# Performance work log

Measured on AMD Instinct MI355X. Metric: run time of the kernel, lower is better.

Reference implementation:

```python
import jax, jax.numpy as jnp
import numpy as np

EMBED_DIM = 1024
NUM_HEADS = 16
N_POS = 2048
BATCH = 4


def setup_inputs() -> dict:
    key = jax.random.key(0)
    k_x, k_w1, k_b1, k_wo, k_bo = jax.random.split(key, 5)
    s1 = 1.0 / np.sqrt(EMBED_DIM)
    x = jax.random.normal(k_x, (BATCH, N_POS, EMBED_DIM), dtype=jnp.float32)
    # torch Linear weights stored as [in, out] for x @ W + b
    W_qkv = jax.random.uniform(k_w1, (EMBED_DIM, 3 * EMBED_DIM), dtype=jnp.float32, minval=-s1, maxval=s1)
    b_qkv = jax.random.uniform(k_b1, (3 * EMBED_DIM,), dtype=jnp.float32, minval=-s1, maxval=s1)
    W_o = jax.random.uniform(k_wo, (EMBED_DIM, EMBED_DIM), dtype=jnp.float32, minval=-s1, maxval=s1)
    b_o = jax.random.uniform(k_bo, (EMBED_DIM,), dtype=jnp.float32, minval=-s1, maxval=s1)
    return {"x": x, "W_qkv": W_qkv, "b_qkv": b_qkv, "W_o": W_o, "b_o": b_o}


def reference(x, W_qkv, b_qkv, W_o, b_o):
    B, N, C = x.shape
    H = NUM_HEADS
    d_k = C // H
    qkv = x @ W_qkv + b_qkv                       # [B, N, 3C]
    q, k, v = jnp.split(qkv, 3, axis=-1)
    q = q.reshape(B, N, H, d_k).transpose(0, 2, 1, 3)  # [B, H, N, d_k]
    k = k.reshape(B, N, H, d_k).transpose(0, 2, 1, 3)
    v = v.reshape(B, N, H, d_k).transpose(0, 2, 1, 3)
    scores = jnp.einsum('bhqd,bhkd->bhqk', q, k) * (1.0 / np.sqrt(d_k))
    causal = jnp.tril(jnp.ones((N, N), dtype=bool))
    scores = jnp.where(causal, scores, -jnp.inf)
    attn = jax.nn.softmax(scores, axis=-1)
    out = jnp.einsum('bhqk,bhkd->bhqd', attn, v)  # [B, H, N, d_k]
    out = out.transpose(0, 2, 1, 3).reshape(B, N, C)
    return out @ W_o + b_o
```

## Files before the change

kernel.cpp:

```cpp
#include <hip/hip_runtime.h>
#include <hip/hip_bf16.h>

typedef __attribute__((ext_vector_type(8))) __bf16 bf16x8;
typedef __attribute__((ext_vector_type(4))) float f32x4;
typedef __attribute__((ext_vector_type(16))) float f32x16;
typedef __attribute__((ext_vector_type(4))) unsigned short u16x4;
typedef __attribute__((ext_vector_type(8))) unsigned short u16x8;
typedef unsigned short u16;

#define MFMA16 __builtin_amdgcn_mfma_f32_16x16x32_bf16
#define MFMA32 __builtin_amdgcn_mfma_f32_32x32x16_bf16

#if __has_builtin(__builtin_amdgcn_exp2f)
#define EXP2F __builtin_amdgcn_exp2f
#else
#define EXP2F(x) __expf((x) * 0.69314718056f)
#endif

__device__ inline u16 f32_to_bf16_bits(float f) {
    unsigned u = __builtin_bit_cast(unsigned, f);
    unsigned r = u + 0x7FFFu + ((u >> 16) & 1u);
    return (u16)(r >> 16);
}
__device__ inline u16 f32_to_bf16_fast(float f) {
    unsigned u = __builtin_bit_cast(unsigned, f);
    return (u16)((u + 0x8000u) >> 16);
}

__device__ inline void g2l16(const void* g, void* l) {
    __builtin_amdgcn_global_load_lds(
        (const __attribute__((address_space(1))) unsigned int*)g,
        (__attribute__((address_space(3))) unsigned int*)l,
        16, 0, 0);
}

__global__ void cvt_bf16_kernel(const float* __restrict__ in, u16* __restrict__ out, int n) {
    int i = (blockIdx.x * 256 + threadIdx.x) * 4;
    if (i >= n) return;
    f32x4 v = *(const f32x4*)&in[i];
    u16x4 r;
#pragma unroll
    for (int j = 0; j < 4; ++j) r[j] = f32_to_bf16_bits(v[j]);
    *(u16x4*)&out[i] = r;
}

__global__ __launch_bounds__(256) void cvt_t_kernel(const float* __restrict__ W,
                                                    u16* __restrict__ WT, int K, int N) {
    const int w = threadIdx.x >> 6, l = threadIdx.x & 63;
    const int n = blockIdx.x * 64 + l;
    const int k0 = blockIdx.y * 32 + w * 8;
    u16x8 r;
#pragma unroll
    for (int i = 0; i < 8; ++i)
        r[i] = f32_to_bf16_bits(W[(size_t)(k0 + i) * N + n]);
    *(u16x8*)&WT[(size_t)n * K + k0] = r;
}

template <int STORE_BF16>
__global__ __launch_bounds__(256) void gemm_nt(
    const u16* __restrict__ A, const u16* __restrict__ BT,
    const float* __restrict__ bias, void* __restrict__ Cv,
    int M, int N, int K, int qcols, float qscale)
{
    __shared__ __align__(16) u16 As[128 * 64];
    __shared__ __align__(16) u16 Bs[128 * 64];
    const int tid = threadIdx.x;
    const int w = tid >> 6, l = tid & 63;
    const int lr = l & 15, lh = l >> 4;
    const int wr = (w >> 1) * 64, wc = (w & 1) * 64;
    const int m0 = blockIdx.y * 128, n0 = blockIdx.x * 128;

    f32x4 acc[4][4];
#pragma unroll
    for (int m = 0; m < 4; ++m)
#pragma unroll
        for (int n = 0; n < 4; ++n) acc[m][n] = (f32x4)(0.0f);

    for (int k0 = 0; k0 < K; k0 += 64) {
        __syncthreads();
#pragma unroll
        for (int p = 0; p < 4; ++p) {
            int f = p * 256 + tid;
            int r = f >> 3, kk = (f & 7) << 3;
            g2l16(A + (size_t)(m0 + r) * K + (k0 + kk), &As[(p * 4 + w) * 512]);
            g2l16(BT + (size_t)(n0 + r) * K + (k0 + kk), &Bs[(p * 4 + w) * 512]);
        }
        __syncthreads();
#pragma unroll
        for (int ks = 0; ks < 2; ++ks) {
            bf16x8 af[4], bfr[4];
#pragma unroll
            for (int m = 0; m < 4; ++m)
                af[m] = *(const bf16x8*)&As[(wr + m * 16 + lr) * 64 + ks * 32 + lh * 8];
#pragma unroll
            for (int n = 0; n < 4; ++n)
                bfr[n] = *(const bf16x8*)&Bs[(wc + n * 16 + lr) * 64 + ks * 32 + lh * 8];
#pragma unroll
            for (int m = 0; m < 4; ++m)
#pragma unroll
                for (int n = 0; n < 4; ++n)
                    acc[m][n] = MFMA16(af[m], bfr[n], acc[m][n], 0, 0, 0);
        }
    }

#pragma unroll
    for (int m = 0; m < 4; ++m) {
        int row = m0 + wr + m * 16 + lh * 4;
#pragma unroll
        for (int n = 0; n < 4; ++n) {
            int col = n0 + wc + n * 16 + lr;
            float bs = bias[col];
            float sc = (col < qcols) ? qscale : 1.0f;
#pragma unroll
            for (int j = 0; j < 4; ++j) {
                float v = (acc[m][n][j] + bs) * sc;
                if (STORE_BF16)
                    ((u16*)Cv)[(size_t)(row + j) * N + col] = f32_to_bf16_bits(v);
                else
                    ((float*)Cv)[(size_t)(row + j) * N + col] = v;
            }
        }
    }
}

__global__ __launch_bounds__(512, 2) void attn_kernel(
    const u16* __restrict__ qkv, u16* __restrict__ ctx)
{
    __shared__ __align__(16) u16 SM[32768];

    const int bid = blockIdx.x;
    const int xcd = bid & 7, jj = bid >> 3;
    const int bh = xcd * 8 + (jj >> 2);
    const int pr = jj & 3;
    const int b = bh >> 4, h = bh & 15;
    const size_t rowbase = (size_t)b * 2048;
    const int tid = threadIdx.x, w = tid >> 6, l = tid & 63;
    const int lq = l & 31, lk = l >> 5;
    u16* const PL = SM + 16384 + w * 2048;

    const int rstage = w * 8 + (l >> 3);
    const int cstage = l & 7;
    const int kchunk = cstage ^ (l >> 3);

    bf16x8 vreg;

#pragma unroll
    for (int pass = 0; pass < 2; ++pass) {
        const int qt = pass ? (7 - pr) : pr;
        const int q0 = qt * 256;
        const int nt = 4 * qt + 4;
        const int qbase = q0 + w * 32;

        const u16* qp = qkv + (rowbase + qbase + lq) * 3072 + h * 64 + lk * 8;
        bf16x8 qf[4];
#pragma unroll
        for (int j = 0; j < 4; ++j) qf[j] = *(const bf16x8*)(qp + j * 16);

        f32x16 ot[2];
#pragma unroll
        for (int dt = 0; dt < 2; ++dt) ot[dt] = (f32x16)(0.0f);
        float m_run = -3e38f, l_run = 0.0f;

        __syncthreads();
        g2l16(qkv + (rowbase + rstage) * 3072 + 1024 + h * 64 + kchunk * 8, SM + w * 512);
        vreg = *(const bf16x8*)(qkv + (rowbase + rstage) * 3072 + 2048 + h * 64 + cstage * 8);
        asm volatile("s_waitcnt vmcnt(0)" ::: "memory");
#pragma unroll
        for (int i = 0; i < 8; ++i) {
            const int d = cstage * 8 + i;
            SM[8192 + (((d * 64 + rstage) ^ (((i ^ cstage) & 7) << 3)))] = ((const u16*)&vreg)[i];
        }
        __syncthreads();

        for (int t = 0; t < nt; ++t) {
            const int c = t & 1;
            const int kb = t * 64;
            u16* const Kb = SM + (c ? 4096 : 0);
            u16* const Vb = SM + 8192 + (c ? 4096 : 0);

            if (t + 1 < nt) {
                const int kb2 = kb + 64;
                g2l16(qkv + (rowbase + kb2 + rstage) * 3072 + 1024 + h * 64 + kchunk * 8,
                      SM + (c ? 0 : 4096) + w * 512);
                vreg = *(const bf16x8*)(qkv + (rowbase + kb2 + rstage) * 3072 + 2048 + h * 64 + cstage * 8);
            }

            if (kb <= qbase + 31) {
                bf16x8 kf[2][4];
#pragma unroll
                for (int kt = 0; kt < 2; ++kt)
#pragma unroll
                    for (int j = 0; j < 4; ++j)
                        kf[kt][j] = *(const bf16x8*)&Kb[((kt * 32 + lq) * 64 + j * 16 + lk * 8) ^ ((lq & 7) << 3)];

                f32x16 sf[2];
                __builtin_amdgcn_s_setprio(1);
#pragma unroll
                for (int kt = 0; kt < 2; ++kt) {
                    f32x16 z = (f32x16)(0.0f);
#pragma unroll
                    for (int j = 0; j < 4; ++j) z = MFMA32(kf[kt][j], qf[j], z, 0, 0, 0);
                    sf[kt] = z;
                }
                __builtin_amdgcn_s_setprio(0);

                float mt = -3e38f;
                if (kb + 63 > qbase) {
                    const int qrow = qbase + lq;
#pragma unroll
                    for (int kt = 0; kt < 2; ++kt)
#pragma unroll
                        for (int r = 0; r < 16; ++r) {
                            const int key = kb + kt * 32 + (r & 3) + 8 * (r >> 2) + 4 * lk;
                            float v = sf[kt][r];
                            if (key > qrow) v = -3e38f;
                            sf[kt][r] = v;
                            mt = fmaxf(mt, v);
                        }
                } else {
#pragma unroll
                    for (int kt = 0; kt < 2; ++kt)
#pragma unroll
                        for (int r = 0; r < 16; ++r) mt = fmaxf(mt, sf[kt][r]);
                }
                mt = fmaxf(mt, __shfl_xor(mt, 32));

                const bool defer = __all(mt <= m_run + 16.0f);
                float mn = m_run;
                if (!defer) {
                    mn = fmaxf(m_run, mt);
                    const float alpha = EXP2F(m_run - mn);
                    m_run = mn;
                    l_run *= alpha;
#pragma unroll
                    for (int dt = 0; dt < 2; ++dt)
#pragma unroll
                        for (int r = 0; r < 16; ++r) ot[dt][r] *= alpha;
                }
                float rs = 0.0f;
#pragma unroll
                for (int kt = 0; kt < 2; ++kt)
#pragma unroll
                    for (int r = 0; r < 16; ++r) {
                        const float pp = EXP2F(sf[kt][r] - mn);
                        sf[kt][r] = pp;
                        rs += pp;
                    }
                rs += __shfl_xor(rs, 32);
                l_run += rs;

#pragma unroll
                for (int kt = 0; kt < 2; ++kt)
#pragma unroll
                    for (int rg = 0; rg < 4; ++rg) {
                        u16x4 pk;
#pragma unroll
                        for (int j2 = 0; j2 < 4; ++j2) pk[j2] = f32_to_bf16_fast(sf[kt][rg * 4 + j2]);
                        *(u16x4*)&PL[((lq * 64) + (kt * 32 + rg * 8 + lk * 4)) ^ ((lq & 7) << 3)] = pk;
                    }

                __builtin_amdgcn_s_setprio(1);
#pragma unroll
                for (int k0 = 0; k0 < 4; ++k0) {
                    const bf16x8 pb = *(const bf16x8*)&PL[((lq * 64) + (k0 * 16 + lk * 8)) ^ ((lq & 7) << 3)];
#pragma unroll
                    for (int dt = 0; dt < 2; ++dt) {
                        const int d = dt * 32 + lq;
                        const int vswz = ((d & 7) ^ (d >> 3)) & 7;
                        const bf16x8 vf = *(const bf16x8*)&Vb[((d * 64) + (k0 * 16 + lk * 8)) ^ (vswz << 3)];
                        ot[dt] = MFMA32(vf, pb, ot[dt], 0, 0, 0);
                    }
                }
                __builtin_amdgcn_s_setprio(0);
            }

            asm volatile("s_waitcnt vmcnt(0)" ::: "memory");
            if (t + 1 < nt) {
                u16* const Vn = SM + 8192 + (c ? 0 : 4096);
#pragma unroll
                for (int i = 0; i < 8; ++i) {
                    const int d = cstage * 8 + i;
                    Vn[((d * 64 + rstage) ^ (((i ^ cstage) & 7) << 3))] = ((const u16*)&vreg)[i];
                }
            }
            __syncthreads();
        }

        u16* const out_l = SM + w * 2176;
        const float inv = 1.0f / l_run;
#pragma unroll
        for (int dt = 0; dt < 2; ++dt)
#pragma unroll
            for (int r = 0; r < 16; ++r) {
                const int d = dt * 32 + (r & 3) + 8 * (r >> 2) + 4 * lk;
                out_l[lq * 68 + d] = f32_to_bf16_bits(ot[dt][r] * inv);
            }
#pragma unroll
        for (int rr = 0; rr < 4; ++rr) {
            const int row = rr * 8 + (l >> 3);
            const bf16x8 v = *(const bf16x8*)&out_l[row * 68 + (l & 7) * 8];
            *(bf16x8*)(ctx + (rowbase + qbase + row) * 1024 + h * 64 + (l & 7) * 8) = v;
        }
    }
}

extern "C" void kernel_launch(void* const* d_in, const int* in_sizes, int n_in,
                              void* d_out, int out_size, void* d_ws, size_t ws_size,
                              hipStream_t stream) {
    const float* x      = (const float*)d_in[0];
    const float* W_qkv  = (const float*)d_in[1];
    const float* b_qkv  = (const float*)d_in[2];
    const float* W_o    = (const float*)d_in[3];
    const float* b_o    = (const float*)d_in[4];
    float* out = (float*)d_out;

    const int M = 4 * 2048;
    const int C = 1024;
    u16* qkv   = (u16*)d_ws;
    u16* xb    = qkv   + (size_t)M * 3 * C;
    u16* wqkvt = xb    + (size_t)M * C;
    u16* ctx   = wqkvt + (size_t)3 * C * C;
    u16* wot   = ctx   + (size_t)M * C;

    const float SCQ = 0.125f * 1.44269504089f;

    cvt_bf16_kernel<<<(M * C) / (256 * 4), 256, 0, stream>>>(x, xb, M * C);
    cvt_t_kernel<<<dim3(3 * C / 64, C / 32), 256, 0, stream>>>(W_qkv, wqkvt, C, 3 * C);
    cvt_t_kernel<<<dim3(C / 64, C / 32), 256, 0, stream>>>(W_o, wot, C, C);

    gemm_nt<1><<<dim3(3 * C / 128, M / 128), 256, 0, stream>>>(xb, wqkvt, b_qkv, qkv, M, 3 * C, C, C, SCQ);

    attn_kernel<<<256, 512, 0, stream>>>(qkv, ctx);

    gemm_nt<0><<<dim3(C / 128, M / 128), 256, 0, stream>>>(ctx, wot, b_o, out, M, C, C, 0, 1.0f);
}
```

Baseline: 190.2 us.

## Triple-buffer GEMM K-loop with swizzled LDS and XCD-aware block remap

New measurement: 175.7 us. 1.08x faster.

```diff
diff --git a/kernel.cpp b/kernel.cpp
--- a/kernel.cpp
+++ b/kernel.cpp
@@ -60,15 +60,37 @@
 __global__ __launch_bounds__(256) void gemm_nt(
     const u16* __restrict__ A, const u16* __restrict__ BT,
     const float* __restrict__ bias, void* __restrict__ Cv,
-    int M, int N, int K, int qcols, float qscale)
+    int M, int N, int K, int qcols, float qscale, int nbx)
 {
-    __shared__ __align__(16) u16 As[128 * 64];
-    __shared__ __align__(16) u16 Bs[128 * 64];
+    __shared__ __align__(16) u16 SM[24576];
     const int tid = threadIdx.x;
     const int w = tid >> 6, l = tid & 63;
     const int lr = l & 15, lh = l >> 4;
     const int wr = (w >> 1) * 64, wc = (w & 1) * 64;
-    const int m0 = blockIdx.y * 128, n0 = blockIdx.x * 128;
+
+    const int nwg = gridDim.x;
+    const int swz = (blockIdx.x & 7) * (nwg >> 3) + (blockIdx.x >> 3);
+    const int m0 = (swz / nbx) * 128;
+    const int n0 = (swz % nbx) * 128;
+
+    const int NT = K >> 5;
+
+    const int f0 = tid, f1 = 256 + tid;
+    const int r0 = f0 >> 2, r1 = f1 >> 2;
+    const int cs0 = ((f0 & 3) ^ ((r0 >> 1) & 3)) * 8;
+    const int cs1 = ((f1 & 3) ^ ((r1 >> 1) & 3)) * 8;
+    const size_t arow0 = (size_t)(m0 + r0) * K, arow1 = (size_t)(m0 + r1) * K;
+    const size_t brow0 = (size_t)(n0 + r0) * K, brow1 = (size_t)(n0 + r1) * K;
+
+#define STAGE_TILE(t, set)                                                     \
+    do {                                                                       \
+        const int kk_ = (t) * 32;                                              \
+        u16* dst_ = SM + (set) * 8192 + w * 512;                               \
+        g2l16(A + arow0 + kk_ + cs0, dst_);                                    \
+        g2l16(BT + brow0 + kk_ + cs0, dst_ + 4096);                            \
+        g2l16(A + arow1 + kk_ + cs1, dst_ + 2048);                             \
+        g2l16(BT + brow1 + kk_ + cs1, dst_ + 4096 + 2048);                     \
+    } while (0)
 
     f32x4 acc[4][4];
 #pragma unroll
@@ -76,32 +98,41 @@
 #pragma unroll
         for (int n = 0; n < 4; ++n) acc[m][n] = (f32x4)(0.0f);
 
-    for (int k0 = 0; k0 < K; k0 += 64) {
-        __syncthreads();
-#pragma unroll
-        for (int p = 0; p < 4; ++p) {
-            int f = p * 256 + tid;
-            int r = f >> 3, kk = (f & 7) << 3;
-            g2l16(A + (size_t)(m0 + r) * K + (k0 + kk), &As[(p * 4 + w) * 512]);
-            g2l16(BT + (size_t)(n0 + r) * K + (k0 + kk), &Bs[(p * 4 + w) * 512]);
-        }
-        __syncthreads();
-#pragma unroll
-        for (int ks = 0; ks < 2; ++ks) {
-            bf16x8 af[4], bfr[4];
-#pragma unroll
-            for (int m = 0; m < 4; ++m)
-                af[m] = *(const bf16x8*)&As[(wr + m * 16 + lr) * 64 + ks * 32 + lh * 8];
+    STAGE_TILE(0, 0);
+    STAGE_TILE(1, 1);
+    asm volatile("s_waitcnt vmcnt(4) lgkmcnt(0)\n\ts_barrier" ::: "memory");
+
+    const int csw = (lr >> 1) & 3;
+    int s0 = 0, s2 = 2;
+    for (int t = 0; t < NT; ++t) {
+        if (t + 2 < NT) STAGE_TILE(t + 2, s2);
+
+        const u16* As = SM + s0 * 8192;
+        const u16* Bs = As + 4096;
+        bf16x8 af[4], bfr[4];
+#pragma unroll
+        for (int m = 0; m < 4; ++m)
+            af[m] = *(const bf16x8*)&As[(wr + m * 16 + lr) * 32 + ((lh ^ csw) << 3)];
+#pragma unroll
+        for (int n = 0; n < 4; ++n)
+            bfr[n] = *(const bf16x8*)&Bs[(wc + n * 16 + lr) * 32 + ((lh ^ csw) << 3)];
+        __builtin_amdgcn_s_setprio(1);
+#pragma unroll
+        for (int m = 0; m < 4; ++m)
 #pragma unroll
             for (int n = 0; n < 4; ++n)
-                bfr[n] = *(const bf16x8*)&Bs[(wc + n * 16 + lr) * 64 + ks * 32 + lh * 8];
-#pragma unroll
-            for (int m = 0; m < 4; ++m)
-#pragma unroll
-                for (int n = 0; n < 4; ++n)
-                    acc[m][n] = MFMA16(af[m], bfr[n], acc[m][n], 0, 0, 0);
-        }
+                acc[m][n] = MFMA16(af[m], bfr[n], acc[m][n], 0, 0, 0);
+        __builtin_amdgcn_s_setprio(0);
+
+        if (t + 2 < NT)
+            asm volatile("s_waitcnt vmcnt(4) lgkmcnt(0)\n\ts_barrier" ::: "memory");
+        else if (t + 1 < NT)
+            asm volatile("s_waitcnt vmcnt(0) lgkmcnt(0)\n\ts_barrier" ::: "memory");
+
+        s0 = (s0 == 2) ? 0 : s0 + 1;
+        s2 = (s2 == 2) ? 0 : s2 + 1;
     }
+#undef STAGE_TILE
 
 #pragma unroll
     for (int m = 0; m < 4; ++m) {
@@ -328,9 +359,11 @@
     cvt_t_kernel<<<dim3(3 * C / 64, C / 32), 256, 0, stream>>>(W_qkv, wqkvt, C, 3 * C);
     cvt_t_kernel<<<dim3(C / 64, C / 32), 256, 0, stream>>>(W_o, wot, C, C);
 
-    gemm_nt<1><<<dim3(3 * C / 128, M / 128), 256, 0, stream>>>(xb, wqkvt, b_qkv, qkv, M, 3 * C, C, C, SCQ);
+    gemm_nt<1><<<(3 * C / 128) * (M / 128), 256, 0, stream>>>(xb, wqkvt, b_qkv, qkv,
+                                                              M, 3 * C, C, C, SCQ, 3 * C / 128);
 
     attn_kernel<<<256, 512, 0, stream>>>(qkv, ctx);
 
-    gemm_nt<0><<<dim3(C / 128, M / 128), 256, 0, stream>>>(ctx, wot, b_o, out, M, C, C, 0, 1.0f);
-}
+    gemm_nt<0><<<(C / 128) * (M / 128), 256, 0, stream>>>(ctx, wot, b_o, out,
+                                                          M, C, C, 0, 1.0f, C / 128);
+}
```
